# Kernel optimization log

Hardware: AMD Instinct MI355X
Metric: run time of the kernel (lower is better)

Reference implementation:

```python
import jax, jax.numpy as jnp
import numpy as np
from jax import lax

T_DATA = 20000
E_NO = 2000
I_NO = 500
SUB_NO = 16
SYN_B = 3
HID = 256
T_SYN = 200
T_ENC = 80


def _causal_conv(x, kern):
    # x: [T, S] per-subunit drive; kern: [S, K] causal kernels (index = lag)
    S, K = kern.shape
    lhs = jnp.pad(x.T, ((0, 0), (K - 1, 0)))[None]        # [1, S, T+K-1]
    rhs = kern[:, ::-1][:, None, :]                        # flip then correlate == torch conv1d path
    out = lax.conv_general_dilated(lhs, rhs, (1,), 'VALID', feature_group_count=S)
    return out[0].T                                        # [T, S]


def setup_inputs() -> dict:
    key = jax.random.key(0)
    ks = jax.random.split(key, 16)
    V_in = jax.random.normal(ks[0], (T_DATA,), jnp.float32) * 5.0 - 69.0
    S_e = jax.random.bernoulli(ks[1], 0.02, (T_DATA, E_NO)).astype(jnp.float32)
    S_i = jax.random.bernoulli(ks[2], 0.02, (T_DATA, I_NO)).astype(jnp.float32)
    # synapse -> subunit one-hot assignment matrices [sub_no, n_syn]
    C_syn_e = jax.nn.one_hot(jax.random.randint(ks[3], (E_NO,), 0, SUB_NO), SUB_NO, dtype=jnp.float32).T
    C_syn_i = jax.nn.one_hot(jax.random.randint(ks[4], (I_NO,), 0, SUB_NO), SUB_NO, dtype=jnp.float32).T
    # parameters, initialized exactly as in __init__
    K_syn = jnp.stack([jnp.full((SUB_NO, SYN_B), 0.04),
                       jnp.full((SUB_NO, SYN_B), -0.02),
                       jnp.full((SUB_NO, SYN_B), 0.02)], axis=-1)          # [sub, B, 3]
    tau_syn = jnp.tile((jnp.arange(SYN_B, dtype=jnp.float32) + 1.6)[:, None], (1, 3))  # [B, 3]
    delta_syn = jnp.full((SUB_NO, 2), 2.0, jnp.float32)
    enc_bias = jnp.zeros((SUB_NO - 1,), jnp.float32)
    W_in = 2 * T_ENC - 1

    def lin(k, fan_out, fan_in):
        kw, kb = jax.random.split(k)
        s = 1.0 / np.sqrt(fan_in)
        return (jax.random.uniform(kw, (fan_out, fan_in), jnp.float32, -s, s),
                jax.random.uniform(kb, (fan_out,), jnp.float32, -s, s))

    W1, b1 = lin(ks[5], HID, W_in)
    W2, b2 = lin(ks[6], HID, HID)
    W3, b3 = lin(ks[7], HID, HID)
    W4, b4 = lin(ks[8], SUB_NO - 1, HID)
    a1 = jnp.float32(0.25)
    a2 = jnp.float32(0.25)
    a3 = jnp.float32(0.25)
    return dict(V_in=V_in, S_e=S_e, S_i=S_i, C_syn_e=C_syn_e, C_syn_i=C_syn_i,
                K_syn=K_syn, tau_syn=tau_syn, delta_syn=delta_syn, enc_bias=enc_bias,
                W1=W1, b1=b1, a1=a1, W2=W2, b2=b2, a2=a2, W3=W3, b3=b3, a3=a3,
                W4=W4, b4=b4)


def reference(V_in, S_e, S_i, C_syn_e, C_syn_i, K_syn, tau_syn, delta_syn, enc_bias,
              W1, b1, a1, W2, b2, a2, W3, b3, a3, W4, b4):
    T = V_in.shape[0]
    # ---- spike_convolve, fully vectorized over (subunit, basis) ----
    t = jnp.arange(T_SYN, dtype=V_in.dtype)                 # [T_syn]
    d = jnp.exp(delta_syn)                                   # [sub, 2]
    te = jnp.maximum(t[None, :] - d[:, 0:1], 0.0)            # [sub, T_syn]
    ti = jnp.maximum(t[None, :] - d[:, 1:2], 0.0)
    tau = jnp.exp(tau_syn)                                   # [B, 3]
    tte = te[:, None, :] / tau[None, :, 0, None]             # [sub, B, T_syn]
    tti = ti[:, None, :] / tau[None, :, 1, None]
    ker_e = jnp.einsum('sbt,sb->st', tte * jnp.exp(-tte), K_syn[:, :, 0])
    ker_i = jnp.einsum('sbt,sb->st', tti * jnp.exp(-tti), K_syn[:, :, 1])
    in_e = S_e @ C_syn_e.T                                   # [T, sub]
    in_i = S_i @ C_syn_i.T
    S_conv = _causal_conv(in_e, ker_e) + _causal_conv(in_i, ker_i)   # [T, sub]
    # ---- encode: batched sliding-window MLP (replaces per-timestep loop) ----
    W = 2 * T_ENC - 1
    Vpad = jnp.zeros((T + W,), V_in.dtype).at[T_ENC - 1:T_ENC - 1 + T].set(V_in)
    idx = jnp.arange(T)[:, None] + jnp.arange(W)[None, :]    # [T, W]
    win = Vpad[idx]                                          # [T, W]
    prelu = lambda x, a: jnp.where(x >= 0, x, a * x)
    h = prelu(win @ W1.T + b1, a1)
    h = prelu(h @ W2.T + b2, a2)
    h = prelu(h @ W3.T + b3, a3)
    nn_out = h @ W4.T + b4                                   # [T, sub-1]
    return jax.nn.sigmoid(nn_out + S_conv[:, 1:] + enc_bias)
```

## Files before the change

kernel.cpp:

```cpp
#include <hip/hip_runtime.h>
#include <cstdint>
#include <cstddef>

#define T_DATA 20000
#define E_NO 2000
#define I_NO 500
#define SUB_NO 16
#define HID 256
#define T_SYN 200
#define T_ENC 80
#define W_IN 159

typedef __attribute__((ext_vector_type(8))) __bf16 bf16x8;
typedef __attribute__((ext_vector_type(8))) short short8;
typedef __attribute__((ext_vector_type(4))) float floatx4;
typedef __attribute__((ext_vector_type(4))) unsigned int uint4v;
typedef __attribute__((ext_vector_type(2))) unsigned int uint2v;

__device__ __forceinline__ float bf2f(unsigned short u) {
    union { unsigned int i; float f; } v; v.i = ((unsigned int)u) << 16; return v.f;
}
__device__ __forceinline__ unsigned short f2bf(float f) {
    union { float f; unsigned int i; } v; v.f = f;
    unsigned int r = v.i + 0x7FFFu + ((v.i >> 16) & 1u);
    return (unsigned short)(r >> 16);
}
__device__ __forceinline__ float inload(const void* p, int i, int isbf) {
    return isbf ? bf2f(((const unsigned short*)p)[i]) : ((const float*)p)[i];
}

__device__ __forceinline__ int detect_bf(const void* Se, int* sfl) {
    if (threadIdx.x == 0) *sfl = 0;
    __syncthreads();
    const unsigned int* w = (const unsigned int*)Se;
    int la = 0;
    #pragma unroll
    for (int i = 0; i < 4; i++)
        la |= (w[i * 256 + threadIdx.x] & 0xFFFFu) ? 1 : 0;
    if (la) atomicOr(sfl, 1);
    __syncthreads();
    return *sfl;
}

#define OFF_KERE   16u
#define OFF_KERI   12816u
#define OFF_SHE    25616u
#define OFF_SHI    33616u
#define OFF_W1H    35616u
#define OFF_W1L    117536u
#define OFF_W2H    199456u
#define OFF_W2L    330528u
#define OFF_W3H    461600u
#define OFF_W3L    592672u
#define OFF_W4H    723744u
#define OFF_W4L    731424u
#define OFF_INE    739104u
#define OFF_INI    1059104u
#define OFF_SCONV  1379104u

__global__ void k_setup(const void* Se, const void* Ksyn, const void* tau_syn, const void* dly,
                        const void* Ce, const void* Ci,
                        const void* W1, const void* W2, const void* W3, const void* W4,
                        float* ker_e, float* ker_i, unsigned char* sh_e, unsigned char* sh_i,
                        unsigned short* W1h, unsigned short* W1l,
                        unsigned short* W2h, unsigned short* W2l,
                        unsigned short* W3h, unsigned short* W3l,
                        unsigned short* W4h, unsigned short* W4l) {
    __shared__ int sfl;
    int f = detect_bf(Se, &sfl);
    int id = blockIdx.x * 256 + threadIdx.x;
    if (id < 6400) {
        int c = id < 3200 ? 0 : 1;
        int q = id - c * 3200;
        int s = q / 200, j = q - s * 200;
        float d = expf(inload(dly, s * 2 + c, f));
        float tt = fmaxf((float)j - d, 0.0f);
        float acc = 0.f;
        #pragma unroll
        for (int b = 0; b < 3; b++) {
            float tau = expf(inload(tau_syn, b * 3 + c, f));
            float x = tt / tau;
            acc += x * expf(-x) * inload(Ksyn, (s * 3 + b) * 3 + c, f);
        }
        (c == 0 ? ker_e : ker_i)[s * 200 + j] = acc;
    } else if (id < 8400) {
        int e = id - 6400;
        int a = 0;
        for (int s = 0; s < 16; s++) if (inload(Ce, s * E_NO + e, f) > 0.5f) a = s;
        sh_e[e] = (unsigned char)(a * 8);
    } else if (id < 8900) {
        int e = id - 8400;
        int a = 0;
        for (int s = 0; s < 16; s++) if (inload(Ci, s * I_NO + e, f) > 0.5f) a = s;
        sh_i[e] = (unsigned char)(a * 8);
    } else if (id < 49860) {
        int q = id - 8900;
        int n = q / 160, k = q - n * 160;
        float v = (k < W_IN) ? inload(W1, n * W_IN + k, f) : 0.f;
        unsigned short hi = f2bf(v);
        W1h[q] = hi;
        W1l[q] = f2bf(v - bf2f(hi));
    } else if (id < 115396) {
        int q = id - 49860;
        float v = inload(W2, q, f);
        unsigned short hi = f2bf(v);
        W2h[q] = hi;
        W2l[q] = f2bf(v - bf2f(hi));
    } else if (id < 180932) {
        int q = id - 115396;
        float v = inload(W3, q, f);
        unsigned short hi = f2bf(v);
        W3h[q] = hi;
        W3l[q] = f2bf(v - bf2f(hi));
    } else if (id < 184772) {
        int q = id - 180932;
        float v = inload(W4, q, f);
        unsigned short hi = f2bf(v);
        W4h[q] = hi;
        W4l[q] = f2bf(v - bf2f(hi));
    }
}

__device__ __forceinline__ void acc_slot(unsigned int b, unsigned int sh,
                                         unsigned long long& lo, unsigned long long& hi) {
    unsigned int up = sh >> 6;
    unsigned int s6 = sh & 63;
    lo += (unsigned long long)(b & (up ^ 1u)) << s6;
    hi += (unsigned long long)(b & up) << s6;
}

__global__ void __launch_bounds__(256) k_spikes(const void* Se, const void* Si,
                         const unsigned char* sh_e, const unsigned char* sh_i,
                         unsigned char* in_e, unsigned char* in_i) {
    __shared__ int sfl;
    __shared__ __align__(8) unsigned char she[E_NO];
    __shared__ __align__(8) unsigned char shi[I_NO];
    for (int i = threadIdx.x; i < E_NO / 4; i += 256)
        ((unsigned int*)she)[i] = ((const unsigned int*)sh_e)[i];
    for (int i = threadIdx.x; i < I_NO / 4; i += 256)
        ((unsigned int*)shi)[i] = ((const unsigned int*)sh_i)[i];
    int f = detect_bf(Se, &sfl);
    int lane = threadIdx.x & 63;
    int wave = threadIdx.x >> 6;
    int t = blockIdx.x * 4 + wave;
    unsigned long long e0 = 0, e1 = 0, i0 = 0, i1 = 0;
    if (f) {
        const uint4v* re = (const uint4v*)((const unsigned short*)Se + (size_t)t * E_NO);
        #pragma unroll
        for (int it = 0; it < 4; it++) {
            int c = it * 64 + lane;
            if (c < 250) {
                uint4v v = re[c];
                unsigned long long q = *(const unsigned long long*)&she[c * 8];
                #pragma unroll
                for (int w = 0; w < 4; w++) {
                    unsigned int x = v[w];
                    acc_slot((x >> 7) & 1u,  (unsigned int)(q >> (16 * w)) & 0xFFu, e0, e1);
                    acc_slot((x >> 23) & 1u, (unsigned int)(q >> (16 * w + 8)) & 0xFFu, e0, e1);
                }
            }
        }
        const uint2v* ri = (const uint2v*)((const unsigned short*)Si + (size_t)t * I_NO);
        #pragma unroll
        for (int it = 0; it < 2; it++) {
            int c = it * 64 + lane;
            if (c < 125) {
                uint2v v = ri[c];
                unsigned int q = *(const unsigned int*)&shi[c * 4];
                #pragma unroll
                for (int w = 0; w < 2; w++) {
                    unsigned int x = v[w];
                    acc_slot((x >> 7) & 1u,  (q >> (16 * w)) & 0xFFu, i0, i1);
                    acc_slot((x >> 23) & 1u, (q >> (16 * w + 8)) & 0xFFu, i0, i1);
                }
            }
        }
    } else {
        const uint4v* re = (const uint4v*)((const float*)Se + (size_t)t * E_NO);
        #pragma unroll
        for (int it = 0; it < 8; it++) {
            int c = it * 64 + lane;
            if (c < 500) {
                uint4v v = re[c];
                unsigned int q = *(const unsigned int*)&she[c * 4];
                #pragma unroll
                for (int w = 0; w < 4; w++)
                    acc_slot((v[w] >> 23) & 1u, (q >> (8 * w)) & 0xFFu, e0, e1);
            }
        }
        const uint2v* ri = (const uint2v*)((const float*)Si + (size_t)t * I_NO);
        #pragma unroll
        for (int it = 0; it < 4; it++) {
            int c = it * 64 + lane;
            if (c < 250) {
                uint2v v = ri[c];
                unsigned int q = *(const unsigned short*)&shi[c * 2];
                #pragma unroll
                for (int w = 0; w < 2; w++)
                    acc_slot((v[w] >> 23) & 1u, (q >> (8 * w)) & 0xFFu, i0, i1);
            }
        }
    }
    for (int off = 32; off; off >>= 1) {
        e0 += __shfl_xor(e0, off);
        e1 += __shfl_xor(e1, off);
        i0 += __shfl_xor(i0, off);
        i1 += __shfl_xor(i1, off);
    }
    if (lane < 16) {
        unsigned long long a = (lane < 8) ? e0 : e1;
        in_e[(size_t)t * 16 + lane] = (unsigned char)((a >> ((lane & 7) * 8)) & 0xFF);
    } else if (lane < 32) {
        int s = lane - 16;
        unsigned long long a = (s < 8) ? i0 : i1;
        in_i[(size_t)t * 16 + s] = (unsigned char)((a >> ((s & 7) * 8)) & 0xFF);
    }
}

__global__ void __launch_bounds__(256) k_conv(
        const unsigned char* in_e, const unsigned char* in_i,
        const float* ker_e, const float* ker_i, float* S_conv) {
    __shared__ float se[263 * 17];
    __shared__ float si[263 * 17];
    __shared__ float ke[16 * 201];
    __shared__ float ki[16 * 201];
    int t0 = blockIdx.x * 64;
    for (int idx = threadIdx.x; idx < 263 * 4; idx += 256) {
        int r = idx >> 2, wi = idx & 3;
        int t = t0 - 199 + r;
        unsigned int ve = 0, vi = 0;
        if (t >= 0 && t < T_DATA) {
            ve = ((const unsigned int*)in_e)[t * 4 + wi];
            vi = ((const unsigned int*)in_i)[t * 4 + wi];
        }
        #pragma unroll
        for (int b = 0; b < 4; b++) {
            se[r * 17 + wi * 4 + b] = (float)((ve >> (8 * b)) & 0xFF);
            si[r * 17 + wi * 4 + b] = (float)((vi >> (8 * b)) & 0xFF);
        }
    }
    for (int idx = threadIdx.x; idx < 3200; idx += 256) {
        int s = idx / 200, j = idx - s * 200;
        ke[s * 201 + j] = ker_e[idx];
        ki[s * 201 + j] = ker_i[idx];
    }
    __syncthreads();
    int s = threadIdx.x & 15, g4 = (threadIdx.x >> 4) * 4;
    float a0 = 0.f, a1 = 0.f, a2 = 0.f, a3 = 0.f;
    float w0 = se[(g4 + 199) * 17 + s], w1 = se[(g4 + 200) * 17 + s];
    float w2 = se[(g4 + 201) * 17 + s], w3 = se[(g4 + 202) * 17 + s];
    float x0 = si[(g4 + 199) * 17 + s], x1 = si[(g4 + 200) * 17 + s];
    float x2 = si[(g4 + 201) * 17 + s], x3 = si[(g4 + 202) * 17 + s];
    #pragma unroll 4
    for (int j = 0; j < 200; j++) {
        float kej = ke[s * 201 + j];
        float kij = ki[s * 201 + j];
        a0 += w0 * kej + x0 * kij;
        a1 += w1 * kej + x1 * kij;
        a2 += w2 * kej + x2 * kij;
        a3 += w3 * kej + x3 * kij;
        int lr = g4 + 198 - j; lr = lr < 0 ? 0 : lr;
        float nw = se[lr * 17 + s], nx = si[lr * 17 + s];
        w3 = w2; w2 = w1; w1 = w0; w0 = nw;
        x3 = x2; x2 = x1; x1 = x0; x0 = nx;
    }
    int tb = t0 + g4;
    if (tb + 0 < T_DATA) S_conv[(size_t)(tb + 0) * 16 + s] = a0;
    if (tb + 1 < T_DATA) S_conv[(size_t)(tb + 1) * 16 + s] = a1;
    if (tb + 2 < T_DATA) S_conv[(size_t)(tb + 2) * 16 + s] = a2;
    if (tb + 3 < T_DATA) S_conv[(size_t)(tb + 3) * 16 + s] = a3;
}

template<bool BF>
__device__ __forceinline__ void mlp_body(
    const void* V,
    const unsigned short* W1h, const unsigned short* W1l, const void* b1, const void* a1p,
    const unsigned short* W2h, const unsigned short* W2l, const void* b2, const void* a2p,
    const unsigned short* W3h, const unsigned short* W3l, const void* b3, const void* a3p,
    const unsigned short* W4h, const unsigned short* W4l, const void* b4,
    const void* encb, const float* S_conv, void* out,
    unsigned short* Ahi, unsigned short* Alo)
{
    int tid = threadIdx.x;
    int lane = tid & 63, wave = tid >> 6;
    int lm = lane & 15, quad = lane >> 4;
    int t0 = blockIdx.x * 64;

    auto ld = [&](const void* p, int i) -> float {
        return BF ? bf2f(((const unsigned short*)p)[i]) : ((const float*)p)[i];
    };

    for (int idx = tid; idx < 64 * 160; idx += 256) {
        int m = idx / 160, k = idx - m * 160;
        int tg = t0 + m + k - (T_ENC - 1);
        float v = 0.f;
        if (k < W_IN && tg >= 0 && tg < T_DATA) v = ld(V, tg);
        unsigned short hi = f2bf(v);
        int col = (((k >> 3) ^ (m & 31)) << 3) | (k & 7);
        Ahi[m * 256 + col] = hi;
        if (!BF) Alo[m * 256 + col] = f2bf(v - bf2f(hi));
    }
    __syncthreads();

    floatx4 acc[4][4];
    auto aoff = [&](int mt, int ks) {
        int arow = mt * 16 + lm;
        return arow * 256 + ((((ks << 2) | quad) ^ (arow & 31)) << 3);
    };

    auto epi = [&](const void* bias, float alpha) {
        __syncthreads();
        #pragma unroll
        for (int mt = 0; mt < 4; mt++) {
            #pragma unroll
            for (int nt = 0; nt < 4; nt++) {
                int cn = wave * 64 + nt * 16 + lm;
                float bb = ld(bias, cn);
                #pragma unroll
                for (int j = 0; j < 4; j++) {
                    int row = mt * 16 + quad * 4 + j;
                    float h = acc[mt][nt][j] + bb;
                    h = (h >= 0.f) ? h : alpha * h;
                    unsigned short hi = f2bf(h);
                    int col = (((cn >> 3) ^ (row & 31)) << 3) | (cn & 7);
                    Ahi[row * 256 + col] = hi;
                    if (!BF) Alo[row * 256 + col] = f2bf(h - bf2f(hi));
                }
            }
        }
        __syncthreads();
    };

    floatx4 z = {0.f, 0.f, 0.f, 0.f};
    {
        #pragma unroll
        for (int mt = 0; mt < 4; mt++)
            #pragma unroll
            for (int nt = 0; nt < 4; nt++) acc[mt][nt] = z;
        if (BF) {
            bf16x8 Bh[5][4];
            #pragma unroll
            for (int ks = 0; ks < 5; ks++)
                #pragma unroll
                for (int nt = 0; nt < 4; nt++)
                    Bh[ks][nt] = *(const bf16x8*)(W1h + (size_t)(wave * 64 + nt * 16 + lm) * 160 + ks * 32 + quad * 8);
            #pragma unroll
            for (int ks = 0; ks < 5; ks++) {
                bf16x8 a[4];
                #pragma unroll
                for (int mt = 0; mt < 4; mt++) a[mt] = *(const bf16x8*)&Ahi[aoff(mt, ks)];
                #pragma unroll
                for (int nt = 0; nt < 4; nt++)
                    #pragma unroll
                    for (int mt = 0; mt < 4; mt++)
                        acc[mt][nt] = __builtin_amdgcn_mfma_f32_16x16x32_bf16(a[mt], Bh[ks][nt], acc[mt][nt], 0, 0, 0);
            }
        } else {
            for (int ks = 0; ks < 5; ks++) {
                bf16x8 ah[4], al[4];
                #pragma unroll
                for (int mt = 0; mt < 4; mt++) {
                    ah[mt] = *(const bf16x8*)&Ahi[aoff(mt, ks)];
                    al[mt] = *(const bf16x8*)&Alo[aoff(mt, ks)];
                }
                #pragma unroll
                for (int nt = 0; nt < 4; nt++) {
                    size_t bo = (size_t)(wave * 64 + nt * 16 + lm) * 160 + ks * 32 + quad * 8;
                    bf16x8 bh = *(const bf16x8*)(W1h + bo);
                    bf16x8 bl = *(const bf16x8*)(W1l + bo);
                    #pragma unroll
                    for (int mt = 0; mt < 4; mt++) {
                        acc[mt][nt] = __builtin_amdgcn_mfma_f32_16x16x32_bf16(ah[mt], bh, acc[mt][nt], 0, 0, 0);
                        acc[mt][nt] = __builtin_amdgcn_mfma_f32_16x16x32_bf16(al[mt], bh, acc[mt][nt], 0, 0, 0);
                        acc[mt][nt] = __builtin_amdgcn_mfma_f32_16x16x32_bf16(ah[mt], bl, acc[mt][nt], 0, 0, 0);
                    }
                }
            }
        }
        epi(b1, ld(a1p, 0));
    }
    const unsigned short* Whs[2] = {W2h, W3h};
    const unsigned short* Wls[2] = {W2l, W3l};
    const void* bs[2] = {b2, b3};
    const void* as_[2] = {a2p, a3p};
    for (int l = 0; l < 2; l++) {
        #pragma unroll
        for (int mt = 0; mt < 4; mt++)
            #pragma unroll
            for (int nt = 0; nt < 4; nt++) acc[mt][nt] = z;
        const unsigned short* Wh = Whs[l];
        const unsigned short* Wl = Wls[l];
        if (BF) {
            bf16x8 Bh[8][4];
            #pragma unroll
            for (int ks = 0; ks < 8; ks++)
                #pragma unroll
                for (int nt = 0; nt < 4; nt++)
                    Bh[ks][nt] = *(const bf16x8*)(Wh + (size_t)(wave * 64 + nt * 16 + lm) * 256 + ks * 32 + quad * 8);
            #pragma unroll
            for (int ks = 0; ks < 8; ks++) {
                bf16x8 a[4];
                #pragma unroll
                for (int mt = 0; mt < 4; mt++) a[mt] = *(const bf16x8*)&Ahi[aoff(mt, ks)];
                #pragma unroll
                for (int nt = 0; nt < 4; nt++)
                    #pragma unroll
                    for (int mt = 0; mt < 4; mt++)
                        acc[mt][nt] = __builtin_amdgcn_mfma_f32_16x16x32_bf16(a[mt], Bh[ks][nt], acc[mt][nt], 0, 0, 0);
            }
        } else {
            for (int ks = 0; ks < 8; ks++) {
                bf16x8 ah[4], al[4];
                #pragma unroll
                for (int mt = 0; mt < 4; mt++) {
                    ah[mt] = *(const bf16x8*)&Ahi[aoff(mt, ks)];
                    al[mt] = *(const bf16x8*)&Alo[aoff(mt, ks)];
                }
                #pragma unroll
                for (int nt = 0; nt < 4; nt++) {
                    size_t bo = (size_t)(wave * 64 + nt * 16 + lm) * 256 + ks * 32 + quad * 8;
                    bf16x8 bh = *(const bf16x8*)(Wh + bo);
                    bf16x8 bl = *(const bf16x8*)(Wl + bo);
                    #pragma unroll
                    for (int mt = 0; mt < 4; mt++) {
                        acc[mt][nt] = __builtin_amdgcn_mfma_f32_16x16x32_bf16(ah[mt], bh, acc[mt][nt], 0, 0, 0);
                        acc[mt][nt] = __builtin_amdgcn_mfma_f32_16x16x32_bf16(al[mt], bh, acc[mt][nt], 0, 0, 0);
                        acc[mt][nt] = __builtin_amdgcn_mfma_f32_16x16x32_bf16(ah[mt], bl, acc[mt][nt], 0, 0, 0);
                    }
                }
            }
        }
        epi(bs[l], ld(as_[l], 0));
    }
    {
        int mt = wave;
        short8 z8 = {0, 0, 0, 0, 0, 0, 0, 0};
        bf16x8 bz = __builtin_bit_cast(bf16x8, z8);
        floatx4 a4 = z;
        #pragma unroll
        for (int ks = 0; ks < 8; ks++) {
            bf16x8 ah = *(const bf16x8*)&Ahi[aoff(mt, ks)];
            bf16x8 bh = bz;
            if (lm < 15)
                bh = *(const bf16x8*)(W4h + (size_t)lm * 256 + ks * 32 + quad * 8);
            a4 = __builtin_amdgcn_mfma_f32_16x16x32_bf16(ah, bh, a4, 0, 0, 0);
            if (!BF) {
                bf16x8 al = *(const bf16x8*)&Alo[aoff(mt, ks)];
                bf16x8 bl = bz;
                if (lm < 15)
                    bl = *(const bf16x8*)(W4l + (size_t)lm * 256 + ks * 32 + quad * 8);
                a4 = __builtin_amdgcn_mfma_f32_16x16x32_bf16(al, bh, a4, 0, 0, 0);
                a4 = __builtin_amdgcn_mfma_f32_16x16x32_bf16(ah, bl, a4, 0, 0, 0);
            }
        }
        if (lm < 15) {
            float bb = ld(b4, lm) + ld(encb, lm);
            #pragma unroll
            for (int j = 0; j < 4; j++) {
                int row = mt * 16 + quad * 4 + j;
                int t = t0 + row;
                if (t < T_DATA) {
                    float x = a4[j] + bb + S_conv[(size_t)t * 16 + lm + 1];
                    x = fminf(fmaxf(x, -40.f), 40.f);
                    float sg = 1.f / (1.f + expf(-x));
                    if (BF) ((unsigned short*)out)[(size_t)t * 15 + lm] = f2bf(sg);
                    else    ((float*)out)[(size_t)t * 15 + lm] = sg;
                }
            }
        }
    }
}

__global__ void __launch_bounds__(256, 2) k_mlp(
    const void* Se, const void* V,
    const unsigned short* W1h, const unsigned short* W1l, const void* b1, const void* a1p,
    const unsigned short* W2h, const unsigned short* W2l, const void* b2, const void* a2p,
    const unsigned short* W3h, const unsigned short* W3l, const void* b3, const void* a3p,
    const unsigned short* W4h, const unsigned short* W4l, const void* b4,
    const void* encb, const float* S_conv, void* out) {
    __shared__ __align__(16) unsigned short Ahi[64 * 256];
    __shared__ __align__(16) unsigned short Alo[64 * 256];
    __shared__ int sfl;
    int f = detect_bf(Se, &sfl);
    if (f)
        mlp_body<true>(V, W1h, W1l, b1, a1p, W2h, W2l, b2, a2p, W3h, W3l, b3, a3p,
                       W4h, W4l, b4, encb, S_conv, out, Ahi, Alo);
    else
        mlp_body<false>(V, W1h, W1l, b1, a1p, W2h, W2l, b2, a2p, W3h, W3l, b3, a3p,
                        W4h, W4l, b4, encb, S_conv, out, Ahi, Alo);
}

extern "C" void kernel_launch(void* const* d_in, const int* in_sizes, int n_in,
                              void* d_out, int out_size, void* d_ws, size_t ws_size,
                              hipStream_t stream) {
    const void* V    = d_in[0];
    const void* Se   = d_in[1];
    const void* Si   = d_in[2];
    const void* Ce   = d_in[3];
    const void* Ci   = d_in[4];
    const void* Ksyn = d_in[5];
    const void* tau  = d_in[6];
    const void* dly  = d_in[7];
    const void* encb = d_in[8];
    const void* W1   = d_in[9];
    const void* b1   = d_in[10];
    const void* a1   = d_in[11];
    const void* W2   = d_in[12];
    const void* b2   = d_in[13];
    const void* a2   = d_in[14];
    const void* W3   = d_in[15];
    const void* b3   = d_in[16];
    const void* a3   = d_in[17];
    const void* W4   = d_in[18];
    const void* b4   = d_in[19];

    char* w = (char*)d_ws;
    float* ker_e = (float*)(w + OFF_KERE);
    float* ker_i = (float*)(w + OFF_KERI);
    unsigned char* sh_e = (unsigned char*)(w + OFF_SHE);
    unsigned char* sh_i = (unsigned char*)(w + OFF_SHI);
    unsigned short* W1h = (unsigned short*)(w + OFF_W1H);
    unsigned short* W1l = (unsigned short*)(w + OFF_W1L);
    unsigned short* W2h = (unsigned short*)(w + OFF_W2H);
    unsigned short* W2l = (unsigned short*)(w + OFF_W2L);
    unsigned short* W3h = (unsigned short*)(w + OFF_W3H);
    unsigned short* W3l = (unsigned short*)(w + OFF_W3L);
    unsigned short* W4h = (unsigned short*)(w + OFF_W4H);
    unsigned short* W4l = (unsigned short*)(w + OFF_W4L);
    unsigned char* in_e = (unsigned char*)(w + OFF_INE);
    unsigned char* in_i = (unsigned char*)(w + OFF_INI);
    float* S_conv = (float*)(w + OFF_SCONV);

    k_setup<<<722, 256, 0, stream>>>(Se, Ksyn, tau, dly, Ce, Ci, W1, W2, W3, W4,
                                     ker_e, ker_i, sh_e, sh_i,
                                     W1h, W1l, W2h, W2l, W3h, W3l, W4h, W4l);
    k_spikes<<<5000, 256, 0, stream>>>(Se, Si, sh_e, sh_i, in_e, in_i);
    k_conv<<<313, 256, 0, stream>>>(in_e, in_i, ker_e, ker_i, S_conv);
    k_mlp<<<313, 256, 0, stream>>>(Se, V, W1h, W1l, b1, a1, W2h, W2l, b2, a2,
                                   W3h, W3l, b3, a3, W4h, W4l, b4,
                                   encb, S_conv, d_out);
}
```

Measured before the change: 373.2 us.

## Merge setup and spike kernels; fuse causal conv into MLP kernel via shared memory

Cuts the pipeline from four launches to two. Setup work and spike binning now run as separate block ranges of one front kernel, and each spike block rebuilds the synapse-to-subunit shift table itself instead of reading it from a prior pass. The causal convolution now runs at the start of the MLP kernel, reusing its shared-memory buffer, so the S_conv round trip through global memory and one launch go away. The cost is redundant Ce/Ci scans in every spike block and more per-block work before the MLP starts.

```diff
diff --git a/kernel.cpp b/kernel.cpp
--- a/kernel.cpp
+++ b/kernel.cpp
@@ -44,82 +44,16 @@
 
 #define OFF_KERE   16u
 #define OFF_KERI   12816u
-#define OFF_SHE    25616u
-#define OFF_SHI    33616u
-#define OFF_W1H    35616u
-#define OFF_W1L    117536u
-#define OFF_W2H    199456u
-#define OFF_W2L    330528u
-#define OFF_W3H    461600u
-#define OFF_W3L    592672u
-#define OFF_W4H    723744u
-#define OFF_W4L    731424u
-#define OFF_INE    739104u
-#define OFF_INI    1059104u
-#define OFF_SCONV  1379104u
-
-__global__ void k_setup(const void* Se, const void* Ksyn, const void* tau_syn, const void* dly,
-                        const void* Ce, const void* Ci,
-                        const void* W1, const void* W2, const void* W3, const void* W4,
-                        float* ker_e, float* ker_i, unsigned char* sh_e, unsigned char* sh_i,
-                        unsigned short* W1h, unsigned short* W1l,
-                        unsigned short* W2h, unsigned short* W2l,
-                        unsigned short* W3h, unsigned short* W3l,
-                        unsigned short* W4h, unsigned short* W4l) {
-    __shared__ int sfl;
-    int f = detect_bf(Se, &sfl);
-    int id = blockIdx.x * 256 + threadIdx.x;
-    if (id < 6400) {
-        int c = id < 3200 ? 0 : 1;
-        int q = id - c * 3200;
-        int s = q / 200, j = q - s * 200;
-        float d = expf(inload(dly, s * 2 + c, f));
-        float tt = fmaxf((float)j - d, 0.0f);
-        float acc = 0.f;
-        #pragma unroll
-        for (int b = 0; b < 3; b++) {
-            float tau = expf(inload(tau_syn, b * 3 + c, f));
-            float x = tt / tau;
-            acc += x * expf(-x) * inload(Ksyn, (s * 3 + b) * 3 + c, f);
-        }
-        (c == 0 ? ker_e : ker_i)[s * 200 + j] = acc;
-    } else if (id < 8400) {
-        int e = id - 6400;
-        int a = 0;
-        for (int s = 0; s < 16; s++) if (inload(Ce, s * E_NO + e, f) > 0.5f) a = s;
-        sh_e[e] = (unsigned char)(a * 8);
-    } else if (id < 8900) {
-        int e = id - 8400;
-        int a = 0;
-        for (int s = 0; s < 16; s++) if (inload(Ci, s * I_NO + e, f) > 0.5f) a = s;
-        sh_i[e] = (unsigned char)(a * 8);
-    } else if (id < 49860) {
-        int q = id - 8900;
-        int n = q / 160, k = q - n * 160;
-        float v = (k < W_IN) ? inload(W1, n * W_IN + k, f) : 0.f;
-        unsigned short hi = f2bf(v);
-        W1h[q] = hi;
-        W1l[q] = f2bf(v - bf2f(hi));
-    } else if (id < 115396) {
-        int q = id - 49860;
-        float v = inload(W2, q, f);
-        unsigned short hi = f2bf(v);
-        W2h[q] = hi;
-        W2l[q] = f2bf(v - bf2f(hi));
-    } else if (id < 180932) {
-        int q = id - 115396;
-        float v = inload(W3, q, f);
-        unsigned short hi = f2bf(v);
-        W3h[q] = hi;
-        W3l[q] = f2bf(v - bf2f(hi));
-    } else if (id < 184772) {
-        int q = id - 180932;
-        float v = inload(W4, q, f);
-        unsigned short hi = f2bf(v);
-        W4h[q] = hi;
-        W4l[q] = f2bf(v - bf2f(hi));
-    }
-}
+#define OFF_W1H    25616u
+#define OFF_W1L    107536u
+#define OFF_W2H    189456u
+#define OFF_W2L    320528u
+#define OFF_W3H    451600u
+#define OFF_W3L    582672u
+#define OFF_W4H    713744u
+#define OFF_W4L    721424u
+#define OFF_INE    729104u
+#define OFF_INI    1049104u
 
 __device__ __forceinline__ void acc_slot(unsigned int b, unsigned int sh,
                                          unsigned long long& lo, unsigned long long& hi) {
@@ -129,146 +63,170 @@
     hi += (unsigned long long)(b & up) << s6;
 }
 
-__global__ void __launch_bounds__(256) k_spikes(const void* Se, const void* Si,
-                         const unsigned char* sh_e, const unsigned char* sh_i,
-                         unsigned char* in_e, unsigned char* in_i) {
+#define SPIKE_BLOCKS 1250
+#define SETUP_ITEMS  182272
+#define SETUP_BLOCKS 712
+
+__global__ void __launch_bounds__(256) k_front(
+        const void* Se, const void* Si, const void* Ce, const void* Ci,
+        const void* Ksyn, const void* tau_syn, const void* dly,
+        const void* W1, const void* W2, const void* W3, const void* W4,
+        float* ker_e, float* ker_i,
+        unsigned short* W1h, unsigned short* W1l,
+        unsigned short* W2h, unsigned short* W2l,
+        unsigned short* W3h, unsigned short* W3l,
+        unsigned short* W4h, unsigned short* W4l,
+        unsigned char* in_e, unsigned char* in_i) {
     __shared__ int sfl;
     __shared__ __align__(8) unsigned char she[E_NO];
     __shared__ __align__(8) unsigned char shi[I_NO];
-    for (int i = threadIdx.x; i < E_NO / 4; i += 256)
-        ((unsigned int*)she)[i] = ((const unsigned int*)sh_e)[i];
-    for (int i = threadIdx.x; i < I_NO / 4; i += 256)
-        ((unsigned int*)shi)[i] = ((const unsigned int*)sh_i)[i];
-    int f = detect_bf(Se, &sfl);
-    int lane = threadIdx.x & 63;
-    int wave = threadIdx.x >> 6;
-    int t = blockIdx.x * 4 + wave;
-    unsigned long long e0 = 0, e1 = 0, i0 = 0, i1 = 0;
-    if (f) {
-        const uint4v* re = (const uint4v*)((const unsigned short*)Se + (size_t)t * E_NO);
+    int tid = threadIdx.x;
+
+    if (blockIdx.x < SPIKE_BLOCKS) {
+        if (tid == 0) sfl = 0;
+        __syncthreads();
+        {
+            const unsigned int* w = (const unsigned int*)Se;
+            int la = 0;
+            #pragma unroll
+            for (int i = 0; i < 4; i++)
+                la |= (w[i * 256 + tid] & 0xFFFFu) ? 1 : 0;
+            if (la) atomicOr(&sfl, 1);
+        }
+        __syncthreads();
+        int f = sfl;
+        for (int e = tid; e < E_NO; e += 256) {
+            int a = 0;
+            for (int s = 0; s < 16; s++) if (inload(Ce, s * E_NO + e, f) > 0.5f) a = s;
+            she[e] = (unsigned char)(a * 8);
+        }
+        for (int e = tid; e < I_NO; e += 256) {
+            int a = 0;
+            for (int s = 0; s < 16; s++) if (inload(Ci, s * I_NO + e, f) > 0.5f) a = s;
+            shi[e] = (unsigned char)(a * 8);
+        }
+        __syncthreads();
+        int lane = tid & 63, wave = tid >> 6;
         #pragma unroll
-        for (int it = 0; it < 4; it++) {
-            int c = it * 64 + lane;
-            if (c < 250) {
-                uint4v v = re[c];
-                unsigned long long q = *(const unsigned long long*)&she[c * 8];
-                #pragma unroll
-                for (int w = 0; w < 4; w++) {
-                    unsigned int x = v[w];
-                    acc_slot((x >> 7) & 1u,  (unsigned int)(q >> (16 * w)) & 0xFFu, e0, e1);
-                    acc_slot((x >> 23) & 1u, (unsigned int)(q >> (16 * w + 8)) & 0xFFu, e0, e1);
-                }
-            }
-        }
-        const uint2v* ri = (const uint2v*)((const unsigned short*)Si + (size_t)t * I_NO);
-        #pragma unroll
-        for (int it = 0; it < 2; it++) {
-            int c = it * 64 + lane;
-            if (c < 125) {
-                uint2v v = ri[c];
-                unsigned int q = *(const unsigned int*)&shi[c * 4];
-                #pragma unroll
-                for (int w = 0; w < 2; w++) {
-                    unsigned int x = v[w];
-                    acc_slot((x >> 7) & 1u,  (q >> (16 * w)) & 0xFFu, i0, i1);
-                    acc_slot((x >> 23) & 1u, (q >> (16 * w + 8)) & 0xFFu, i0, i1);
-                }
+        for (int j = 0; j < 4; j++) {
+            int t = blockIdx.x * 16 + wave * 4 + j;
+            unsigned long long e0 = 0, e1 = 0, i0 = 0, i1 = 0;
+            if (f) {
+                const uint4v* re = (const uint4v*)((const unsigned short*)Se + (size_t)t * E_NO);
+                #pragma unroll
+                for (int it = 0; it < 4; it++) {
+                    int c = it * 64 + lane;
+                    if (c < 250) {
+                        uint4v v = re[c];
+                        unsigned long long q = *(const unsigned long long*)&she[c * 8];
+                        #pragma unroll
+                        for (int w = 0; w < 4; w++) {
+                            unsigned int x = v[w];
+                            acc_slot((x >> 7) & 1u,  (unsigned int)(q >> (16 * w)) & 0xFFu, e0, e1);
+                            acc_slot((x >> 23) & 1u, (unsigned int)(q >> (16 * w + 8)) & 0xFFu, e0, e1);
+                        }
+                    }
+                }
+                const uint2v* ri = (const uint2v*)((const unsigned short*)Si + (size_t)t * I_NO);
+                #pragma unroll
+                for (int it = 0; it < 2; it++) {
+                    int c = it * 64 + lane;
+                    if (c < 125) {
+                        uint2v v = ri[c];
+                        unsigned int q = *(const unsigned int*)&shi[c * 4];
+                        #pragma unroll
+                        for (int w = 0; w < 2; w++) {
+                            unsigned int x = v[w];
+                            acc_slot((x >> 7) & 1u,  (q >> (16 * w)) & 0xFFu, i0, i1);
+                            acc_slot((x >> 23) & 1u, (q >> (16 * w + 8)) & 0xFFu, i0, i1);
+                        }
+                    }
+                }
+            } else {
+                const uint4v* re = (const uint4v*)((const float*)Se + (size_t)t * E_NO);
+                #pragma unroll
+                for (int it = 0; it < 8; it++) {
+                    int c = it * 64 + lane;
+                    if (c < 500) {
+                        uint4v v = re[c];
+                        unsigned int q = *(const unsigned int*)&she[c * 4];
+                        #pragma unroll
+                        for (int w = 0; w < 4; w++)
+                            acc_slot((v[w] >> 23) & 1u, (q >> (8 * w)) & 0xFFu, e0, e1);
+                    }
+                }
+                const uint2v* ri = (const uint2v*)((const float*)Si + (size_t)t * I_NO);
+                #pragma unroll
+                for (int it = 0; it < 4; it++) {
+                    int c = it * 64 + lane;
+                    if (c < 250) {
+                        uint2v v = ri[c];
+                        unsigned int q = *(const unsigned short*)&shi[c * 2];
+                        #pragma unroll
+                        for (int w = 0; w < 2; w++)
+                            acc_slot((v[w] >> 23) & 1u, (q >> (8 * w)) & 0xFFu, i0, i1);
+                    }
+                }
+            }
+            for (int off = 32; off; off >>= 1) {
+                e0 += __shfl_xor(e0, off);
+                e1 += __shfl_xor(e1, off);
+                i0 += __shfl_xor(i0, off);
+                i1 += __shfl_xor(i1, off);
+            }
+            if (lane < 16) {
+                unsigned long long a = (lane < 8) ? e0 : e1;
+                in_e[(size_t)t * 16 + lane] = (unsigned char)((a >> ((lane & 7) * 8)) & 0xFF);
+            } else if (lane < 32) {
+                int s = lane - 16;
+                unsigned long long a = (s < 8) ? i0 : i1;
+                in_i[(size_t)t * 16 + s] = (unsigned char)((a >> ((s & 7) * 8)) & 0xFF);
             }
         }
     } else {
-        const uint4v* re = (const uint4v*)((const float*)Se + (size_t)t * E_NO);
-        #pragma unroll
-        for (int it = 0; it < 8; it++) {
-            int c = it * 64 + lane;
-            if (c < 500) {
-                uint4v v = re[c];
-                unsigned int q = *(const unsigned int*)&she[c * 4];
-                #pragma unroll
-                for (int w = 0; w < 4; w++)
-                    acc_slot((v[w] >> 23) & 1u, (q >> (8 * w)) & 0xFFu, e0, e1);
-            }
-        }
-        const uint2v* ri = (const uint2v*)((const float*)Si + (size_t)t * I_NO);
-        #pragma unroll
-        for (int it = 0; it < 4; it++) {
-            int c = it * 64 + lane;
-            if (c < 250) {
-                uint2v v = ri[c];
-                unsigned int q = *(const unsigned short*)&shi[c * 2];
-                #pragma unroll
-                for (int w = 0; w < 2; w++)
-                    acc_slot((v[w] >> 23) & 1u, (q >> (8 * w)) & 0xFFu, i0, i1);
-            }
+        int f = detect_bf(Se, &sfl);
+        int id = (blockIdx.x - SPIKE_BLOCKS) * 256 + tid;
+        if (id < 6400) {
+            int c = id < 3200 ? 0 : 1;
+            int q = id - c * 3200;
+            int s = q / 200, j = q - s * 200;
+            float d = expf(inload(dly, s * 2 + c, f));
+            float tt = fmaxf((float)j - d, 0.0f);
+            float acc = 0.f;
+            #pragma unroll
+            for (int b = 0; b < 3; b++) {
+                float tau = expf(inload(tau_syn, b * 3 + c, f));
+                float x = tt / tau;
+                acc += x * expf(-x) * inload(Ksyn, (s * 3 + b) * 3 + c, f);
+            }
+            (c == 0 ? ker_e : ker_i)[s * 200 + j] = acc;
+        } else if (id < 47360) {
+            int q = id - 6400;
+            int n = q / 160, k = q - n * 160;
+            float v = (k < W_IN) ? inload(W1, n * W_IN + k, f) : 0.f;
+            unsigned short hi = f2bf(v);
+            W1h[q] = hi;
+            W1l[q] = f2bf(v - bf2f(hi));
+        } else if (id < 112896) {
+            int q = id - 47360;
+            float v = inload(W2, q, f);
+            unsigned short hi = f2bf(v);
+            W2h[q] = hi;
+            W2l[q] = f2bf(v - bf2f(hi));
+        } else if (id < 178432) {
+            int q = id - 112896;
+            float v = inload(W3, q, f);
+            unsigned short hi = f2bf(v);
+            W3h[q] = hi;
+            W3l[q] = f2bf(v - bf2f(hi));
+        } else if (id < 182272) {
+            int q = id - 178432;
+            float v = inload(W4, q, f);
+            unsigned short hi = f2bf(v);
+            W4h[q] = hi;
+            W4l[q] = f2bf(v - bf2f(hi));
         }
     }
-    for (int off = 32; off; off >>= 1) {
-        e0 += __shfl_xor(e0, off);
-        e1 += __shfl_xor(e1, off);
-        i0 += __shfl_xor(i0, off);
-        i1 += __shfl_xor(i1, off);
-    }
-    if (lane < 16) {
-        unsigned long long a = (lane < 8) ? e0 : e1;
-        in_e[(size_t)t * 16 + lane] = (unsigned char)((a >> ((lane & 7) * 8)) & 0xFF);
-    } else if (lane < 32) {
-        int s = lane - 16;
-        unsigned long long a = (s < 8) ? i0 : i1;
-        in_i[(size_t)t * 16 + s] = (unsigned char)((a >> ((s & 7) * 8)) & 0xFF);
-    }
-}
-
-__global__ void __launch_bounds__(256) k_conv(
-        const unsigned char* in_e, const unsigned char* in_i,
-        const float* ker_e, const float* ker_i, float* S_conv) {
-    __shared__ float se[263 * 17];
-    __shared__ float si[263 * 17];
-    __shared__ float ke[16 * 201];
-    __shared__ float ki[16 * 201];
-    int t0 = blockIdx.x * 64;
-    for (int idx = threadIdx.x; idx < 263 * 4; idx += 256) {
-        int r = idx >> 2, wi = idx & 3;
-        int t = t0 - 199 + r;
-        unsigned int ve = 0, vi = 0;
-        if (t >= 0 && t < T_DATA) {
-            ve = ((const unsigned int*)in_e)[t * 4 + wi];
-            vi = ((const unsigned int*)in_i)[t * 4 + wi];
-        }
-        #pragma unroll
-        for (int b = 0; b < 4; b++) {
-            se[r * 17 + wi * 4 + b] = (float)((ve >> (8 * b)) & 0xFF);
-            si[r * 17 + wi * 4 + b] = (float)((vi >> (8 * b)) & 0xFF);
-        }
-    }
-    for (int idx = threadIdx.x; idx < 3200; idx += 256) {
-        int s = idx / 200, j = idx - s * 200;
-        ke[s * 201 + j] = ker_e[idx];
-        ki[s * 201 + j] = ker_i[idx];
-    }
-    __syncthreads();
-    int s = threadIdx.x & 15, g4 = (threadIdx.x >> 4) * 4;
-    float a0 = 0.f, a1 = 0.f, a2 = 0.f, a3 = 0.f;
-    float w0 = se[(g4 + 199) * 17 + s], w1 = se[(g4 + 200) * 17 + s];
-    float w2 = se[(g4 + 201) * 17 + s], w3 = se[(g4 + 202) * 17 + s];
-    float x0 = si[(g4 + 199) * 17 + s], x1 = si[(g4 + 200) * 17 + s];
-    float x2 = si[(g4 + 201) * 17 + s], x3 = si[(g4 + 202) * 17 + s];
-    #pragma unroll 4
-    for (int j = 0; j < 200; j++) {
-        float kej = ke[s * 201 + j];
-        float kij = ki[s * 201 + j];
-        a0 += w0 * kej + x0 * kij;
-        a1 += w1 * kej + x1 * kij;
-        a2 += w2 * kej + x2 * kij;
-        a3 += w3 * kej + x3 * kij;
-        int lr = g4 + 198 - j; lr = lr < 0 ? 0 : lr;
-        float nw = se[lr * 17 + s], nx = si[lr * 17 + s];
-        w3 = w2; w2 = w1; w1 = w0; w0 = nw;
-        x3 = x2; x2 = x1; x1 = x0; x0 = nx;
-    }
-    int tb = t0 + g4;
-    if (tb + 0 < T_DATA) S_conv[(size_t)(tb + 0) * 16 + s] = a0;
-    if (tb + 1 < T_DATA) S_conv[(size_t)(tb + 1) * 16 + s] = a1;
-    if (tb + 2 < T_DATA) S_conv[(size_t)(tb + 2) * 16 + s] = a2;
-    if (tb + 3 < T_DATA) S_conv[(size_t)(tb + 3) * 16 + s] = a3;
 }
 
 template<bool BF>
@@ -278,7 +236,7 @@
     const unsigned short* W2h, const unsigned short* W2l, const void* b2, const void* a2p,
     const unsigned short* W3h, const unsigned short* W3l, const void* b3, const void* a3p,
     const unsigned short* W4h, const unsigned short* W4l, const void* b4,
-    const void* encb, const float* S_conv, void* out,
+    const void* encb, const float* sc, void* out,
     unsigned short* Ahi, unsigned short* Alo)
 {
     int tid = threadIdx.x;
@@ -460,7 +418,7 @@
                 int row = mt * 16 + quad * 4 + j;
                 int t = t0 + row;
                 if (t < T_DATA) {
-                    float x = a4[j] + bb + S_conv[(size_t)t * 16 + lm + 1];
+                    float x = a4[j] + bb + sc[row * 16 + lm + 1];
                     x = fminf(fmaxf(x, -40.f), 40.f);
                     float sg = 1.f / (1.f + expf(-x));
                     if (BF) ((unsigned short*)out)[(size_t)t * 15 + lm] = f2bf(sg);
@@ -471,23 +429,81 @@
     }
 }
 
-__global__ void __launch_bounds__(256, 2) k_mlp(
+__global__ void __launch_bounds__(256, 2) k_back(
     const void* Se, const void* V,
+    const unsigned char* in_e, const unsigned char* in_i,
+    const float* ker_e, const float* ker_i,
     const unsigned short* W1h, const unsigned short* W1l, const void* b1, const void* a1p,
     const unsigned short* W2h, const unsigned short* W2l, const void* b2, const void* a2p,
     const unsigned short* W3h, const unsigned short* W3l, const void* b3, const void* a3p,
     const unsigned short* W4h, const unsigned short* W4l, const void* b4,
-    const void* encb, const float* S_conv, void* out) {
-    __shared__ __align__(16) unsigned short Ahi[64 * 256];
-    __shared__ __align__(16) unsigned short Alo[64 * 256];
+    const void* encb, void* out) {
+    __shared__ __align__(16) char smem[65536];
+    __shared__ __align__(16) float sc[64 * 16];
     __shared__ int sfl;
     int f = detect_bf(Se, &sfl);
+    int tid = threadIdx.x;
+    int t0 = blockIdx.x * 64;
+
+    {
+        float* se = (float*)smem;
+        float* si = se + 263 * 17;
+        float* ke = si + 263 * 17;
+        float* ki = ke + 16 * 201;
+        for (int idx = tid; idx < 263 * 4; idx += 256) {
+            int r = idx >> 2, wi = idx & 3;
+            int t = t0 - 199 + r;
+            unsigned int ve = 0, vi = 0;
+            if (t >= 0 && t < T_DATA) {
+                ve = ((const unsigned int*)in_e)[t * 4 + wi];
+                vi = ((const unsigned int*)in_i)[t * 4 + wi];
+            }
+            #pragma unroll
+            for (int b = 0; b < 4; b++) {
+                se[r * 17 + wi * 4 + b] = (float)((ve >> (8 * b)) & 0xFF);
+                si[r * 17 + wi * 4 + b] = (float)((vi >> (8 * b)) & 0xFF);
+            }
+        }
+        for (int idx = tid; idx < 3200; idx += 256) {
+            int s = idx / 200, j = idx - s * 200;
+            ke[s * 201 + j] = ker_e[idx];
+            ki[s * 201 + j] = ker_i[idx];
+        }
+        __syncthreads();
+        int s = tid & 15, g4 = (tid >> 4) * 4;
+        float a0 = 0.f, a1 = 0.f, a2 = 0.f, a3 = 0.f;
+        float w0 = se[(g4 + 199) * 17 + s], w1 = se[(g4 + 200) * 17 + s];
+        float w2 = se[(g4 + 201) * 17 + s], w3 = se[(g4 + 202) * 17 + s];
+        float x0 = si[(g4 + 199) * 17 + s], x1 = si[(g4 + 200) * 17 + s];
+        float x2 = si[(g4 + 201) * 17 + s], x3 = si[(g4 + 202) * 17 + s];
+        #pragma unroll 4
+        for (int j = 0; j < 200; j++) {
+            float kej = ke[s * 201 + j];
+            float kij = ki[s * 201 + j];
+            a0 += w0 * kej + x0 * kij;
+            a1 += w1 * kej + x1 * kij;
+            a2 += w2 * kej + x2 * kij;
+            a3 += w3 * kej + x3 * kij;
+            int lr = g4 + 198 - j; lr = lr < 0 ? 0 : lr;
+            float nw = se[lr * 17 + s], nx = si[lr * 17 + s];
+            w3 = w2; w2 = w1; w1 = w0; w0 = nw;
+            x3 = x2; x2 = x1; x1 = x0; x0 = nx;
+        }
+        sc[(g4 + 0) * 16 + s] = a0;
+        sc[(g4 + 1) * 16 + s] = a1;
+        sc[(g4 + 2) * 16 + s] = a2;
+        sc[(g4 + 3) * 16 + s] = a3;
+        __syncthreads();
+    }
+
+    unsigned short* Ahi = (unsigned short*)smem;
+    unsigned short* Alo = Ahi + 64 * 256;
     if (f)
         mlp_body<true>(V, W1h, W1l, b1, a1p, W2h, W2l, b2, a2p, W3h, W3l, b3, a3p,
-                       W4h, W4l, b4, encb, S_conv, out, Ahi, Alo);
+                       W4h, W4l, b4, encb, sc, out, Ahi, Alo);
     else
         mlp_body<false>(V, W1h, W1l, b1, a1p, W2h, W2l, b2, a2p, W3h, W3l, b3, a3p,
-                        W4h, W4l, b4, encb, S_conv, out, Ahi, Alo);
+                        W4h, W4l, b4, encb, sc, out, Ahi, Alo);
 }
 
 extern "C" void kernel_launch(void* const* d_in, const int* in_sizes, int n_in,
@@ -517,8 +533,6 @@
     char* w = (char*)d_ws;
     float* ker_e = (float*)(w + OFF_KERE);
     float* ker_i = (float*)(w + OFF_KERI);
-    unsigned char* sh_e = (unsigned char*)(w + OFF_SHE);
-    unsigned char* sh_i = (unsigned char*)(w + OFF_SHI);
     unsigned short* W1h = (unsigned short*)(w + OFF_W1H);
     unsigned short* W1l = (unsigned short*)(w + OFF_W1L);
     unsigned short* W2h = (unsigned short*)(w + OFF_W2H);
@@ -529,14 +543,12 @@
     unsigned short* W4l = (unsigned short*)(w + OFF_W4L);
     unsigned char* in_e = (unsigned char*)(w + OFF_INE);
     unsigned char* in_i = (unsigned char*)(w + OFF_INI);
-    float* S_conv = (float*)(w + OFF_SCONV);
-
-    k_setup<<<722, 256, 0, stream>>>(Se, Ksyn, tau, dly, Ce, Ci, W1, W2, W3, W4,
-                                     ker_e, ker_i, sh_e, sh_i,
-                                     W1h, W1l, W2h, W2l, W3h, W3l, W4h, W4l);
-    k_spikes<<<5000, 256, 0, stream>>>(Se, Si, sh_e, sh_i, in_e, in_i);
-    k_conv<<<313, 256, 0, stream>>>(in_e, in_i, ker_e, ker_i, S_conv);
-    k_mlp<<<313, 256, 0, stream>>>(Se, V, W1h, W1l, b1, a1, W2h, W2l, b2, a2,
-                                   W3h, W3l, b3, a3, W4h, W4l, b4,
-                                   encb, S_conv, d_out);
-}
+
+    k_front<<<SPIKE_BLOCKS + SETUP_BLOCKS, 256, 0, stream>>>(
+        Se, Si, Ce, Ci, Ksyn, tau, dly, W1, W2, W3, W4,
+        ker_e, ker_i, W1h, W1l, W2h, W2l, W3h, W3l, W4h, W4l, in_e, in_i);
+    k_back<<<313, 256, 0, stream>>>(
+        Se, V, in_e, in_i, ker_e, ker_i,
+        W1h, W1l, b1, a1, W2h, W2l, b2, a2, W3h, W3l, b3, a3,
+        W4h, W4l, b4, encb, d_out);
+}
```

After: 381.4 us. +2.2%, slower.
